# Optimization experiments

Hardware: AMD Instinct MI355X
Metric: run time of the kernel (lower is better)

The kernel has to match this reference:

```python
import jax, jax.numpy as jnp
import numpy as np

B, N, C, H = 2, 2048, 256, 8
HD = C // H
EPS = 1e-5


def _cdist(a, b):
    # a: (B,N,D), b: (B,M,D) -> (B,N,M) euclidean distance (torch.cdist p=2)
    d2 = (jnp.sum(a * a, -1)[:, :, None] + jnp.sum(b * b, -1)[:, None, :]
          - 2.0 * jnp.einsum('bnd,bmd->bnm', a, b))
    return jnp.sqrt(jnp.maximum(d2, 0.0))


def _ln(x, g, b):
    # LayerNorm over last axis
    m = jnp.mean(x, -1, keepdims=True)
    v = jnp.var(x, -1, keepdims=True)
    return (x - m) / jnp.sqrt(v + EPS) * g + b


def _conv1d(x, w, b=None):
    # 1x1 Conv1d: x (B,Cin,N), w (Cout,Cin)
    y = jnp.einsum('oc,bcn->bon', w, x)
    return y if b is None else y + b[:, None]


def setup_inputs() -> dict:
    key = jax.random.key(0)
    ks = jax.random.split(key, 32)
    s = 0.05
    inp = {
        'xyz_A': jax.random.normal(ks[0], (B, N, 3), jnp.float32),
        'featA': jax.random.normal(ks[1], (B, C, N), jnp.float32),
        'xyz_B': jax.random.normal(ks[2], (B, N, 3), jnp.float32),
        'featB': jax.random.normal(ks[3], (B, C, N), jnp.float32),
        # q/k/v projections (Conv1d 1x1)
        'qw': jax.random.normal(ks[4], (C, C), jnp.float32) * s,
        'qb': jnp.zeros((C,), jnp.float32),
        'kw': jax.random.normal(ks[5], (C, C), jnp.float32) * s,
        'kb': jnp.zeros((C,), jnp.float32),
        'vw': jax.random.normal(ks[6], (C, C), jnp.float32) * s,
        'vb': jnp.zeros((C,), jnp.float32),
        # spatial_bias_mlp: Conv2d(1,H/2,1,bias=False) -> BN2d(eval) -> ReLU -> Conv2d(H/2,H,1)
        'sbw1': jax.random.normal(ks[7], (H // 2,), jnp.float32) * s,
        'sbg': jnp.ones((H // 2,), jnp.float32),
        'sbb': jnp.zeros((H // 2,), jnp.float32),
        'sbm': jax.random.normal(ks[8], (H // 2,), jnp.float32) * 0.1,
        'sbv': jax.random.uniform(ks[9], (H // 2,), jnp.float32, 0.5, 1.5),
        'sbw2': jax.random.normal(ks[10], (H, H // 2), jnp.float32) * s,
        'sbb2': jnp.zeros((H,), jnp.float32),
        # dissimilarity projections
        'qdw': jax.random.normal(ks[11], (C, C), jnp.float32) * s,
        'qdb': jnp.zeros((C,), jnp.float32),
        'kdw': jax.random.normal(ks[12], (C, C), jnp.float32) * s,
        'kdb': jnp.zeros((C,), jnp.float32),
        # LayerNorms
        'lin_g': jnp.ones((C,), jnp.float32), 'lin_b': jnp.zeros((C,), jnp.float32),
        'lsim_g': jnp.ones((C,), jnp.float32), 'lsim_b': jnp.zeros((C,), jnp.float32),
        'ldis_g': jnp.ones((C,), jnp.float32), 'ldis_b': jnp.zeros((C,), jnp.float32),
        # fusion MLP: Conv1d(3C,2C,bias=False) -> BN1d(eval) -> ReLU -> Dropout(eval) -> Conv1d(2C,C)
        'fw1': jax.random.normal(ks[13], (2 * C, 3 * C), jnp.float32) * s,
        'fbg': jnp.ones((2 * C,), jnp.float32),
        'fbb': jnp.zeros((2 * C,), jnp.float32),
        'fbm': jax.random.normal(ks[14], (2 * C,), jnp.float32) * 0.1,
        'fbv': jax.random.uniform(ks[15], (2 * C,), jnp.float32, 0.5, 1.5),
        'fw2': jax.random.normal(ks[16], (C, 2 * C), jnp.float32) * s,
        'fb2': jnp.zeros((C,), jnp.float32),
    }
    return inp


def _forward(xyz_A, featA, xyz_B, featB, qw, qb, kw, kb, vw, vb,
             sbw1, sbg, sbb, sbm, sbv, sbw2, sbb2,
             qdw, qdb, kdw, kdb,
             lin_g, lin_b, lsim_g, lsim_b, ldis_g, ldis_b,
             fw1, fbg, fbb, fbm, fbv, fw2, fb2):
    # Pre-norm of featA over channels
    featA_norm = _ln(featA.transpose(0, 2, 1), lin_g, lin_b).transpose(0, 2, 1)  # (B,C,N)

    # Spatial bias: -cdist -> 1x1 conv (in_ch=1) -> BN(eval) -> ReLU -> 1x1 conv
    dist = _cdist(xyz_A, xyz_B)                                # (B,N,N)
    t = jnp.einsum('o,bnm->bonm', sbw1, -dist)                 # (B,H/2,N,N)
    t = (t - sbm[:, None, None]) / jnp.sqrt(sbv + EPS)[:, None, None]
    t = t * sbg[:, None, None] + sbb[:, None, None]
    t = jax.nn.relu(t)
    spatial_bias = jnp.einsum('oh,bhnm->bonm', sbw2, t) + sbb2[:, None, None]  # (B,H,N,N)

    # Similarity path
    q = _conv1d(featA_norm, qw, qb).reshape(B, H, HD, N).transpose(0, 1, 3, 2)  # (B,H,N,hd)
    k = _conv1d(featB, kw, kb).reshape(B, H, HD, N).transpose(0, 1, 3, 2)
    sim_scores = jnp.einsum('bhnd,bhmd->bhnm', q, k) / (HD ** 0.5) + spatial_bias

    # Dissimilarity path: feature cdist + spatial bias
    qd = _conv1d(featA_norm, qdw, qdb).transpose(0, 2, 1)      # (B,N,C)
    kd = _conv1d(featB, kdw, kdb).transpose(0, 2, 1)
    dissim_scores = _cdist(qd, kd)[:, None] + spatial_bias     # (B,H,N,N)

    sim_w = jax.nn.softmax(sim_scores, -1)
    dis_w = jax.nn.softmax(dissim_scores, -1)

    v = _conv1d(featB, vw, vb).reshape(B, H, HD, N).transpose(0, 1, 3, 2)       # (B,H,N,hd)
    ctx_sim = jnp.einsum('bhnm,bhmd->bhnd', sim_w, v).transpose(0, 1, 3, 2).reshape(B, C, N)
    ctx_sim = _ln(ctx_sim.transpose(0, 2, 1), lsim_g, lsim_b).transpose(0, 2, 1)
    ctx_dis = jnp.einsum('bhnm,bhmd->bhnd', dis_w, v).transpose(0, 1, 3, 2).reshape(B, C, N)
    ctx_dis = _ln(ctx_dis.transpose(0, 2, 1), ldis_g, ldis_b).transpose(0, 2, 1)

    fused = jnp.concatenate([featA_norm, ctx_sim, ctx_dis], axis=1)            # (B,3C,N)
    x = jnp.einsum('oc,bcn->bon', fw1, fused)
    x = (x - fbm[:, None]) / jnp.sqrt(fbv + EPS)[:, None] * fbg[:, None] + fbb[:, None]
    x = jax.nn.relu(x)  # Dropout is identity in eval mode
    out = _conv1d(x, fw2, fb2) + featA  # residual_proj is Identity (in==out)
    return out


def reference(xyz_A, featA, xyz_B, featB, qw, qb, kw, kb, vw, vb,
              sbw1, sbg, sbb, sbm, sbv, sbw2, sbb2,
              qdw, qdb, kdw, kdb,
              lin_g, lin_b, lsim_g, lsim_b, ldis_g, ldis_b,
              fw1, fbg, fbb, fbm, fbv, fw2, fb2):
    return _forward(xyz_A, featA, xyz_B, featB, qw, qb, kw, kb, vw, vb,
                    sbw1, sbg, sbb, sbm, sbv, sbw2, sbb2,
                    qdw, qdb, kdw, kdb,
                    lin_g, lin_b, lsim_g, lsim_b, ldis_g, ldis_b,
                    fw1, fbg, fbb, fbm, fbv, fw2, fb2)
```

## Files before the change

### kernel.cpp

```cpp
#include <hip/hip_runtime.h>

#define B_ 2
#define N_ 2048
#define C_ 256
#define H_ 8
#define HD_ 32
#define EPSf 1e-5f
#define LOG2E 1.4426950408889634f
#define THRv 8.0f

typedef __bf16   bf16x8 __attribute__((ext_vector_type(8)));
typedef float    f32x4  __attribute__((ext_vector_type(4)));
typedef _Float16 f16x4  __attribute__((ext_vector_type(4)));
typedef _Float16 f16x2  __attribute__((ext_vector_type(2)));

static constexpr size_t MB_ = 1024 * 1024;
static constexpr size_t OFF_FANT = 0;
static constexpr size_t OFF_FBT  = 2 * MB_;
static constexpr size_t OFF_QPK  = 4 * MB_;
static constexpr size_t OFF_KPK  = 6 * MB_;
static constexpr size_t OFF_VPK  = 8 * MB_;
static constexpr size_t OFF_QDT  = 10 * MB_;
static constexpr size_t OFF_KDT  = 12 * MB_;
static constexpr size_t OFF_QQ   = 14 * MB_;
static constexpr size_t OFF_KK   = 14 * MB_ + 16 * 1024;
static constexpr size_t OFF_FSD  = 14 * MB_ + 64 * 1024;
static constexpr size_t OFF_PART  = 47 * MB_;
static constexpr size_t OFF_STATM = 55 * MB_;
static constexpr size_t OFF_STATL = 56 * MB_;
static constexpr size_t OFF_CSLN  = 15 * MB_;
static constexpr size_t OFF_CDLN  = 17 * MB_;
static constexpr size_t OFF_X1T   = 19 * MB_;
static constexpr size_t WS_NEED   = 63 * MB_;

__device__ __forceinline__ float rfl(float x){
  return __uint_as_float(__builtin_amdgcn_readfirstlane(__float_as_uint(x)));
}
__device__ __forceinline__ float fexp2(float x){ return __builtin_amdgcn_exp2f(x); }
__device__ __forceinline__ bf16x8 cvt8(const float* p){
  float4 a = *reinterpret_cast<const float4*>(p);
  float4 c = *reinterpret_cast<const float4*>(p + 4);
  bf16x8 r;
  r[0]=(__bf16)a.x; r[1]=(__bf16)a.y; r[2]=(__bf16)a.z; r[3]=(__bf16)a.w;
  r[4]=(__bf16)c.x; r[5]=(__bf16)c.y; r[6]=(__bf16)c.z; r[7]=(__bf16)c.w;
  return r;
}
__device__ __forceinline__ unsigned int packh2(float lo, float hi){
  f16x2 h; h[0] = (_Float16)lo; h[1] = (_Float16)hi;
  return __builtin_bit_cast(unsigned int, h);
}
__device__ __forceinline__ void unpackh2(unsigned int u, float& lo, float& hi){
  f16x2 h = __builtin_bit_cast(f16x2, u);
  lo = (float)h[0]; hi = (float)h[1];
}
__device__ __forceinline__ f16x4 pack4(float a, float b, float c, float d){
  auto lo = __builtin_amdgcn_cvt_pkrtz(a, b);
  auto hi = __builtin_amdgcn_cvt_pkrtz(c, d);
  unsigned long long u = (unsigned long long)__builtin_bit_cast(unsigned int, lo)
      | ((unsigned long long)__builtin_bit_cast(unsigned int, hi) << 32);
  return __builtin_bit_cast(f16x4, u);
}

__global__ __launch_bounds__(256) void prep_kernel(const float* __restrict__ featA,
    const float* __restrict__ featB, __bf16* __restrict__ fanT, __bf16* __restrict__ fbT,
    const float* __restrict__ gam, const float* __restrict__ bet){
  int b = blockIdx.y;
  int t = threadIdx.x;
  __shared__ float sh[9536];
  if (blockIdx.x < 64){
    int n0 = blockIdx.x * 32;
    int nl = t & 31, cg = t >> 5;
    float* tile = sh;
    float* red1 = sh + 8448;
    float* red2 = red1 + 256;
    float* mus  = red2 + 256;
    float* rss  = mus + 32;
    float* gsh  = rss + 32;
    float* bsh  = gsh + 256;
    gsh[t] = gam[t]; bsh[t] = bet[t];
    #pragma unroll
    for (int i = 0; i < 32; i++){
      int c = cg * 32 + i;
      tile[c * 33 + nl] = featA[((size_t)(b * C_ + c)) * N_ + n0 + nl];
    }
    __syncthreads();
    float s1 = 0.f, s2 = 0.f;
    #pragma unroll
    for (int i = 0; i < 32; i++){
      float v = tile[(cg * 32 + i) * 33 + nl];
      s1 += v; s2 += v * v;
    }
    red1[cg * 32 + nl] = s1; red2[cg * 32 + nl] = s2;
    __syncthreads();
    if (t < 32){
      float a = 0.f, q = 0.f;
      #pragma unroll
      for (int i = 0; i < 8; i++){ a += red1[i * 32 + t]; q += red2[i * 32 + t]; }
      float m = a / (float)C_;
      mus[t] = m; rss[t] = rsqrtf(q / (float)C_ - m * m + EPSf);
    }
    __syncthreads();
    float mu = mus[nl], rs = rss[nl];
    size_t obase = ((size_t)(b * N_ + n0 + nl)) * C_;
    #pragma unroll
    for (int i = 0; i < 32; i++){
      int c = cg * 32 + i;
      fanT[obase + c] = (__bf16)((tile[c * 33 + nl] - mu) * rs * gsh[c] + bsh[c]);
    }
  } else {
    int idx = blockIdx.x - 64;
    int n0 = (idx & 31) * 64, c0 = (idx >> 5) * 64;
    float* tile = sh;
    int cl = t >> 6, nl = t & 63;
    #pragma unroll
    for (int i = 0; i < 16; i++)
      tile[(i * 4 + cl) * 65 + nl] = featB[((size_t)(b * C_ + c0 + i * 4 + cl)) * N_ + n0 + nl];
    __syncthreads();
    int nr = t >> 2, cc = (t & 3) * 16;
    alignas(16) __bf16 tmp[16];
    #pragma unroll
    for (int j = 0; j < 16; j++) tmp[j] = (__bf16)tile[(cc + j) * 65 + nr];
    size_t d = ((size_t)(b * N_ + n0 + nr)) * C_ + c0 + cc;
    *reinterpret_cast<uint4*>(&fbT[d])     = *reinterpret_cast<uint4*>(&tmp[0]);
    *reinterpret_cast<uint4*>(&fbT[d + 8]) = *reinterpret_cast<uint4*>(&tmp[8]);
  }
}

__global__ __launch_bounds__(256) void proj_mfma(const __bf16* __restrict__ fanT,
    const __bf16* __restrict__ fbT, __bf16* __restrict__ wsh,
    const float* __restrict__ qw, const float* __restrict__ qb,
    const float* __restrict__ kw, const float* __restrict__ kb,
    const float* __restrict__ vw, const float* __restrict__ vb,
    const float* __restrict__ qdw, const float* __restrict__ qdb,
    const float* __restrict__ kdw, const float* __restrict__ kdb){
  const int p = blockIdx.z % 5, b = blockIdx.z / 5;
  const int t = threadIdx.x, w = t >> 6, lane = t & 63, ln = lane & 15, g = lane >> 4;
  const float *W, *bias;
  const __bf16* X;
  __bf16* Y;
  if (p == 0)      { W = qw;  bias = qb;  X = fanT; Y = wsh + (OFF_QPK - OFF_FANT) / 2; }
  else if (p == 1) { W = kw;  bias = kb;  X = fbT;  Y = wsh + (OFF_KPK - OFF_FANT) / 2; }
  else if (p == 2) { W = vw;  bias = vb;  X = fbT;  Y = wsh + (OFF_VPK - OFF_FANT) / 2; }
  else if (p == 3) { W = qdw; bias = qdb; X = fanT; Y = wsh + (OFF_QDT - OFF_FANT) / 2; }
  else             { W = kdw; bias = kdb; X = fbT;  Y = wsh + (OFF_KDT - OFF_FANT) / 2; }

  f32x4 acc[4];
  #pragma unroll
  for (int i = 0; i < 4; i++) acc[i] = (f32x4){0.f, 0.f, 0.f, 0.f};

  if (p != 2){
    const int n0w = blockIdx.x * 64 + w * 16, o0 = blockIdx.y * 64;
    #pragma unroll
    for (int ks = 0; ks < 8; ks++){
      bf16x8 af = *reinterpret_cast<const bf16x8*>(
          &X[((size_t)(b * N_ + n0w + ln)) * C_ + ks * 32 + g * 8]);
      #pragma unroll
      for (int ot = 0; ot < 4; ot++){
        bf16x8 bf = cvt8(&W[(size_t)(o0 + ot * 16 + ln) * C_ + ks * 32 + g * 8]);
        acc[ot] = __builtin_amdgcn_mfma_f32_16x16x32_bf16(af, bf, acc[ot], 0, 0, 0);
      }
    }
    const float inv = 0.17677669529663687f * LOG2E;
    #pragma unroll
    for (int ot = 0; ot < 4; ot++){
      int o = o0 + ot * 16 + ln;
      float bz = bias[o];
      #pragma unroll
      for (int r = 0; r < 4; r++){
        int n = n0w + g * 4 + r;
        float val = acc[ot][r] + bz;
        if (p == 0){
          val *= inv;
          Y[(((size_t)(b * H_ + (o >> 5))) * N_ + n) * HD_ + (o & 31)] = (__bf16)val;
        } else if (p == 1){
          Y[(((size_t)(b * H_ + (o >> 5))) * N_ + n) * HD_ + (o & 31)] = (__bf16)val;
        } else {
          Y[((size_t)(b * N_ + n)) * C_ + o] = (__bf16)val;
        }
      }
    }
  } else {
    const int o0w = blockIdx.y * 64 + w * 16, n0 = blockIdx.x * 64;
    #pragma unroll
    for (int ks = 0; ks < 8; ks++){
      bf16x8 af = cvt8(&W[(size_t)(o0w + ln) * C_ + ks * 32 + g * 8]);
      #pragma unroll
      for (int nt = 0; nt < 4; nt++){
        bf16x8 bf = *reinterpret_cast<const bf16x8*>(
            &X[((size_t)(b * N_ + n0 + nt * 16 + ln)) * C_ + ks * 32 + g * 8]);
        acc[nt] = __builtin_amdgcn_mfma_f32_16x16x32_bf16(af, bf, acc[nt], 0, 0, 0);
      }
    }
    float bz[4];
    #pragma unroll
    for (int r = 0; r < 4; r++) bz[r] = vb[o0w + g * 4 + r];
    #pragma unroll
    for (int nt = 0; nt < 4; nt++)
      #pragma unroll
      for (int r = 0; r < 4; r++){
        int o = o0w + g * 4 + r, n = n0 + nt * 16 + ln;
        size_t idx = ((size_t)(b * C_ + o)) * N_ + n;
        ((_Float16*)Y)[idx] = (_Float16)(acc[nt][r] + bz[r]);
      }
  }
}

__global__ __launch_bounds__(256) void norms_b(const __bf16* __restrict__ qdT,
    const __bf16* __restrict__ kdT, float* __restrict__ qq, float* __restrict__ kk){
  int b = blockIdx.y, n = blockIdx.x * 64 + (threadIdx.x >> 2), part = threadIdx.x & 3;
  size_t base = ((size_t)(b * N_ + n)) * C_ + part * 64;
  float s1 = 0.f, s2 = 0.f;
  #pragma unroll
  for (int i = 0; i < 8; i++){
    bf16x8 a = *reinterpret_cast<const bf16x8*>(&qdT[base + i * 8]);
    bf16x8 d = *reinterpret_cast<const bf16x8*>(&kdT[base + i * 8]);
    #pragma unroll
    for (int j = 0; j < 8; j++){
      float fa = (float)a[j]; s1 += fa * fa;
      float fd = (float)d[j]; s2 += fd * fd;
    }
  }
  s1 += __shfl_xor(s1, 1); s1 += __shfl_xor(s1, 2);
  s2 += __shfl_xor(s2, 1); s2 += __shfl_xor(s2, 2);
  if (part == 0){ qq[b * N_ + n] = s1; kk[b * N_ + n] = s2; }
}

__global__ __launch_bounds__(256) void pairdist_mfma(const __bf16* __restrict__ qdT,
    const __bf16* __restrict__ kdT, const float* __restrict__ qq,
    const float* __restrict__ kk, const float* __restrict__ xyzA,
    const float* __restrict__ xyzB, unsigned int* __restrict__ fsd){
  const int t = threadIdx.x, w = t >> 6, lane = t & 63, ln = lane & 15, g = lane >> 4;
  const int b = blockIdx.z, n0 = blockIdx.y * 64, n0w = n0 + w * 16, m0 = blockIdx.x * 64;
  __shared__ float4 xa[64], xb[64];
  __shared__ unsigned int sbl[4][16][68];

  if (t < 64){
    const float* p = &xyzA[((size_t)(b * N_ + n0 + t)) * 3];
    xa[t] = make_float4(p[0], p[1], p[2], 0.f);
  } else if (t < 128){
    const float* p = &xyzB[((size_t)(b * N_ + m0 + t - 64)) * 3];
    xb[t - 64] = make_float4(p[0], p[1], p[2], 0.f);
  }
  bf16x8 qfr[8];
  #pragma unroll
  for (int ks = 0; ks < 8; ks++)
    qfr[ks] = *reinterpret_cast<const bf16x8*>(
        &qdT[((size_t)(b * N_ + n0w + ln)) * C_ + ks * 32 + g * 8]);
  float qqv[4];
  #pragma unroll
  for (int r = 0; r < 4; r++) qqv[r] = qq[b * N_ + n0w + g * 4 + r];
  __syncthreads();
  float4 xav[4];
  #pragma unroll
  for (int r = 0; r < 4; r++) xav[r] = xa[w * 16 + g * 4 + r];

  #pragma unroll
  for (int mt = 0; mt < 4; mt++){
    f32x4 a = (f32x4){0.f, 0.f, 0.f, 0.f};
    #pragma unroll
    for (int ks = 0; ks < 8; ks++){
      bf16x8 kfr = *reinterpret_cast<const bf16x8*>(
          &kdT[((size_t)(b * N_ + m0 + mt * 16 + ln)) * C_ + ks * 32 + g * 8]);
      a = __builtin_amdgcn_mfma_f32_16x16x32_bf16(qfr[ks], kfr, a, 0, 0, 0);
    }
    float kkv = kk[b * N_ + m0 + mt * 16 + ln];
    float4 xbv = xb[mt * 16 + ln];
    #pragma unroll
    for (int r = 0; r < 4; r++){
      float d2 = qqv[r] + kkv - 2.f * a[r];
      float fd = sqrtf(fmaxf(d2, 0.f)) * LOG2E;
      float dx = xav[r].x - xbv.x, dy = xav[r].y - xbv.y, dz = xav[r].z - xbv.z;
      float sd = sqrtf(dx * dx + dy * dy + dz * dz);
      sbl[w][g * 4 + r][mt * 16 + ln] = packh2(fd, sd);
    }
  }
  #pragma unroll
  for (int it = 0; it < 4; it++){
    int row = it * 4 + (lane >> 4), cq = lane & 15;
    uint4 v = *reinterpret_cast<const uint4*>(&sbl[w][row][cq * 4]);
    *reinterpret_cast<uint4*>(&fsd[((size_t)(b * N_ + n0w + row)) * N_ + m0 + cq * 4]) = v;
  }
}

struct TileRegs { uint4 fu[4]; bf16x8 kf[4]; };

__device__ __forceinline__ void load_tile(TileRegs& T, const __bf16* kbase,
    const unsigned int* fsdrow, int m0, int ln, int g){
  #pragma unroll
  for (int mt = 0; mt < 4; mt++){
    T.fu[mt] = *reinterpret_cast<const uint4*>(&fsdrow[m0 + mt * 16 + g * 4]);
    T.kf[mt] = *reinterpret_cast<const bf16x8*>(&kbase[(size_t)(m0 + mt * 16 + ln) * HD_ + g * 8]);
  }
}

__device__ __forceinline__ void compute_tile7(const TileRegs& T,
    const _Float16* vbase, int m0, int ln, int g, bf16x8 qf,
    const float* Ac, const float* Bc, const float* W2h, float C0,
    f32x4* os, f32x4* od, float& ms, float& lps, float& md, float& lpd){
  f32x4 sa[4];
  #pragma unroll
  for (int mt = 0; mt < 4; mt++){
    f32x4 z = (f32x4){0.f, 0.f, 0.f, 0.f};
    sa[mt] = __builtin_amdgcn_mfma_f32_16x16x32_bf16(T.kf[mt], qf, z, 0, 0, 0);
  }
  f16x4 vf[2][4];
  #pragma unroll
  for (int mt = 0; mt < 4; mt++)
    #pragma unroll
    for (int dt = 0; dt < 2; dt++)
      vf[dt][mt] = *reinterpret_cast<const f16x4*>(
          &vbase[(size_t)(dt * 16 + ln) * N_ + m0 + mt * 16 + g * 4]);
  f16x4 pAs[4], pAd[4];
  float tss = 0.f, tsd = 0.f, mxs = -3e38f, mxd = -3e38f;
  #pragma unroll
  for (int mt = 0; mt < 4; mt++){
    float ps[4], pd[4];
    #pragma unroll
    for (int r = 0; r < 4; r++){
      unsigned int uu = (r == 0) ? T.fu[mt].x : (r == 1) ? T.fu[mt].y
                      : (r == 2) ? T.fu[mt].z : T.fu[mt].w;
      float fdl, sd;
      unpackh2(uu, fdl, sd);
      float u0 = fmaxf(fmaf(Ac[0], sd, Bc[0]), 0.f);
      float u1 = fmaxf(fmaf(Ac[1], sd, Bc[1]), 0.f);
      float u2 = fmaxf(fmaf(Ac[2], sd, Bc[2]), 0.f);
      float u3 = fmaxf(fmaf(Ac[3], sd, Bc[3]), 0.f);
      float bias = fmaf(W2h[0], u0, fmaf(W2h[1], u1, fmaf(W2h[2], u2, fmaf(W2h[3], u3, C0))));
      float s = sa[mt][r] + bias;
      float d = fdl + bias;
      mxs = fmaxf(mxs, s); mxd = fmaxf(mxd, d);
      ps[r] = fexp2(s - ms); pd[r] = fexp2(d - md);
      tss += ps[r]; tsd += pd[r];
    }
    pAs[mt] = pack4(ps[0], ps[1], ps[2], ps[3]);
    pAd[mt] = pack4(pd[0], pd[1], pd[2], pd[3]);
  }
  bool fs  = !__all(mxs <= ms + THRv);
  bool fdp = !__all(mxd <= md + THRv);
  if (fs || fdp){
    if (fs){
      float mr = fmaxf(mxs, __shfl_xor(mxs, 16));
      mr = fmaxf(mr, __shfl_xor(mr, 32));
      float nms = fmaxf(ms, mr);
      float f = fexp2(ms - nms);
      ms = nms; lps *= f;
      float a0 = __shfl(f, g * 4 + 0), a1 = __shfl(f, g * 4 + 1);
      float a2 = __shfl(f, g * 4 + 2), a3 = __shfl(f, g * 4 + 3);
      #pragma unroll
      for (int dt = 0; dt < 2; dt++){
        os[dt][0] *= a0; os[dt][1] *= a1; os[dt][2] *= a2; os[dt][3] *= a3;
      }
    }
    if (fdp){
      float mr = fmaxf(mxd, __shfl_xor(mxd, 16));
      mr = fmaxf(mr, __shfl_xor(mr, 32));
      float nmd = fmaxf(md, mr);
      float f = fexp2(md - nmd);
      md = nmd; lpd *= f;
      float a0 = __shfl(f, g * 4 + 0), a1 = __shfl(f, g * 4 + 1);
      float a2 = __shfl(f, g * 4 + 2), a3 = __shfl(f, g * 4 + 3);
      #pragma unroll
      for (int dt = 0; dt < 2; dt++){
        od[dt][0] *= a0; od[dt][1] *= a1; od[dt][2] *= a2; od[dt][3] *= a3;
      }
    }
    tss = 0.f; tsd = 0.f;
    #pragma unroll
    for (int mt = 0; mt < 4; mt++){
      float ps[4], pd[4];
      #pragma unroll
      for (int r = 0; r < 4; r++){
        unsigned int uu = (r == 0) ? T.fu[mt].x : (r == 1) ? T.fu[mt].y
                        : (r == 2) ? T.fu[mt].z : T.fu[mt].w;
        float fdl, sd;
        unpackh2(uu, fdl, sd);
        float u0 = fmaxf(fmaf(Ac[0], sd, Bc[0]), 0.f);
        float u1 = fmaxf(fmaf(Ac[1], sd, Bc[1]), 0.f);
        float u2 = fmaxf(fmaf(Ac[2], sd, Bc[2]), 0.f);
        float u3 = fmaxf(fmaf(Ac[3], sd, Bc[3]), 0.f);
        float bias = fmaf(W2h[0], u0, fmaf(W2h[1], u1, fmaf(W2h[2], u2, fmaf(W2h[3], u3, C0))));
        float s = sa[mt][r] + bias;
        float d = fdl + bias;
        ps[r] = fexp2(s - ms); pd[r] = fexp2(d - md);
        tss += ps[r]; tsd += pd[r];
      }
      pAs[mt] = pack4(ps[0], ps[1], ps[2], ps[3]);
      pAd[mt] = pack4(pd[0], pd[1], pd[2], pd[3]);
    }
  }
  lps += tss; lpd += tsd;
  #pragma unroll
  for (int mt = 0; mt < 4; mt++)
    #pragma unroll
    for (int dt = 0; dt < 2; dt++){
      os[dt] = __builtin_amdgcn_mfma_f32_16x16x16f16(pAs[mt], vf[dt][mt], os[dt], 0, 0, 0);
      od[dt] = __builtin_amdgcn_mfma_f32_16x16x16f16(pAd[mt], vf[dt][mt], od[dt], 0, 0, 0);
    }
}

__global__ __launch_bounds__(256, 4) void dual_attn7(
    const __bf16* __restrict__ qpk, const __bf16* __restrict__ kpk,
    const _Float16* __restrict__ vph, const unsigned int* __restrict__ fsd,
    const float* __restrict__ sbw1, const float* __restrict__ sbg, const float* __restrict__ sbb,
    const float* __restrict__ sbm, const float* __restrict__ sbv,
    const float* __restrict__ sbw2, const float* __restrict__ sbb2,
    _Float16* __restrict__ partO, float* __restrict__ statM, float* __restrict__ statL){
  const int t = threadIdx.x, w = t >> 6, lane = t & 63, ln = lane & 15, g = lane >> 4;
  const int h = blockIdx.y;
  const int b = blockIdx.z >> 1, split = blockIdx.z & 1;
  const int nbase = blockIdx.x * 64 + w * 16;
  const int n = nbase + ln;
  const int mstart = split * (N_ / 2);

  float Ac[4], Bc[4], W2h[4];
  #pragma unroll
  for (int j = 0; j < 4; j++){
    float rs = rsqrtf(sbv[j] + EPSf);
    Ac[j]  = rfl(-sbw1[j] * rs * sbg[j]);
    Bc[j]  = rfl(-sbm[j] * rs * sbg[j] + sbb[j]);
    W2h[j] = rfl(sbw2[h * 4 + j]) * LOG2E;
  }
  float C0 = rfl(sbb2[h]) * LOG2E;

  bf16x8 qf = *reinterpret_cast<const bf16x8*>(
      &qpk[(((size_t)(b * H_ + h)) * N_ + n) * HD_ + g * 8]);
  const unsigned int* fsdrow = &fsd[((size_t)(b * N_ + n)) * N_];
  const __bf16* kbase = &kpk[(((size_t)(b * H_ + h)) * N_) * HD_];
  const _Float16* vbase = &vph[((size_t)(b * C_ + h * HD_)) * N_];

  f32x4 os[2], od[2];
  #pragma unroll
  for (int i = 0; i < 2; i++){ os[i] = (f32x4){0.f,0.f,0.f,0.f}; od[i] = (f32x4){0.f,0.f,0.f,0.f}; }
  float ms = -3e38f, lps = 0.f, md = -3e38f, lpd = 0.f;

  TileRegs T;
  for (int i = 0; i < 16; i++){
    int m0 = mstart + i * 64;
    load_tile(T, kbase, fsdrow, m0, ln, g);
    compute_tile7(T, vbase, m0, ln, g, qf, Ac, Bc, W2h, C0, os, od, ms, lps, md, lpd);
  }

  lps += __shfl_xor(lps, 16); lps += __shfl_xor(lps, 32);
  lpd += __shfl_xor(lpd, 16); lpd += __shfl_xor(lpd, 32);
  float is = 1.f / lps, idd = 1.f / lpd;
  float isr[4], idr[4];
  #pragma unroll
  for (int r = 0; r < 4; r++){
    isr[r] = __shfl(is, g * 4 + r);
    idr[r] = __shfl(idd, g * 4 + r);
  }
  #pragma unroll
  for (int dt = 0; dt < 2; dt++)
    #pragma unroll
    for (int r = 0; r < 4; r++){
      int nn = nbase + g * 4 + r;
      int ch = h * HD_ + dt * 16 + ln;
      size_t p0 = (((size_t)(0 * 2 + split) * B_ + b) * N_ + nn) * C_ + ch;
      size_t p1 = (((size_t)(2 + split) * B_ + b) * N_ + nn) * C_ + ch;
      partO[p0] = (_Float16)(os[dt][r] * isr[r]);
      partO[p1] = (_Float16)(od[dt][r] * idr[r]);
    }
  if (lane < 16){
    int nn = nbase + lane;
    size_t s0 = (((size_t)(0 * 2 + split) * B_ + b) * H_ + h) * N_ + nn;
    size_t s1 = (((size_t)(2 + split) * B_ + b) * H_ + h) * N_ + nn;
    statM[s0] = ms; statL[s0] = lps;
    statM[s1] = md; statL[s1] = lpd;
  }
}

__global__ __launch_bounds__(256) void combine_ln(
    const _Float16* __restrict__ partO, const float* __restrict__ statM,
    const float* __restrict__ statL, __bf16* __restrict__ csLN, __bf16* __restrict__ cdLN,
    const float* __restrict__ lsg, const float* __restrict__ lsb,
    const float* __restrict__ ldg, const float* __restrict__ ldb){
  const int path = blockIdx.y;
  const int w = threadIdx.x >> 6, lane = threadIdx.x & 63;
  const size_t row = (size_t)blockIdx.x * 4 + w;
  const int b = (int)(row >> 11), n = (int)(row & (N_ - 1));
  const int h = lane >> 3;
  const float* gg = path ? ldg : lsg;
  const float* bb = path ? ldb : lsb;
  __bf16* dst = path ? cdLN : csLN;

  size_t pb0 = (((size_t)(path * 2 + 0) * B_ + b) * N_ + n) * C_ + lane * 4;
  size_t pb1 = (((size_t)(path * 2 + 1) * B_ + b) * N_ + n) * C_ + lane * 4;
  f16x4 p0 = *reinterpret_cast<const f16x4*>(&partO[pb0]);
  f16x4 p1 = *reinterpret_cast<const f16x4*>(&partO[pb1]);
  size_t sb0 = (((size_t)(path * 2 + 0) * B_ + b) * H_ + h) * N_ + n;
  size_t sb1 = (((size_t)(path * 2 + 1) * B_ + b) * H_ + h) * N_ + n;
  float m0 = statM[sb0], l0 = statL[sb0];
  float m1 = statM[sb1], l1 = statL[sb1];
  float M = fmaxf(m0, m1);
  float w0 = l0 * fexp2(m0 - M), w1 = l1 * fexp2(m1 - M);
  float inv = 1.f / (w0 + w1);
  float o[4];
  #pragma unroll
  for (int j = 0; j < 4; j++)
    o[j] = (w0 * (float)p0[j] + w1 * (float)p1[j]) * inv;

  float s1 = o[0] + o[1] + o[2] + o[3];
  float s2 = o[0]*o[0] + o[1]*o[1] + o[2]*o[2] + o[3]*o[3];
  #pragma unroll
  for (int off = 1; off < 64; off <<= 1){
    s1 += __shfl_xor(s1, off);
    s2 += __shfl_xor(s2, off);
  }
  float mu = s1 / (float)C_;
  float rs = rsqrtf(s2 / (float)C_ - mu * mu + EPSf);
  float4 g4 = *reinterpret_cast<const float4*>(&gg[lane * 4]);
  float4 b4 = *reinterpret_cast<const float4*>(&bb[lane * 4]);
  alignas(8) __bf16 o4[4];
  o4[0] = (__bf16)((o[0] - mu) * rs * g4.x + b4.x);
  o4[1] = (__bf16)((o[1] - mu) * rs * g4.y + b4.y);
  o4[2] = (__bf16)((o[2] - mu) * rs * g4.z + b4.z);
  o4[3] = (__bf16)((o[3] - mu) * rs * g4.w + b4.w);
  *reinterpret_cast<uint2*>(&dst[row * C_ + lane * 4]) = *reinterpret_cast<uint2*>(o4);
}

__global__ __launch_bounds__(256) void fusion1_mfma(const __bf16* __restrict__ fanT,
    const __bf16* __restrict__ csLN, const __bf16* __restrict__ cdLN,
    __bf16* __restrict__ X1T, const float* __restrict__ fw1,
    const float* __restrict__ fbg, const float* __restrict__ fbb,
    const float* __restrict__ fbm, const float* __restrict__ fbv){
  const int t = threadIdx.x, w = t >> 6, lane = t & 63, ln = lane & 15, g = lane >> 4;
  const int b = blockIdx.z, o0 = blockIdx.y * 64, n0w = blockIdx.x * 64 + w * 16;
  f32x4 acc[4];
  #pragma unroll
  for (int i = 0; i < 4; i++) acc[i] = (f32x4){0.f, 0.f, 0.f, 0.f};
  const __bf16* segs[3] = {fanT, csLN, cdLN};
  #pragma unroll
  for (int ks = 0; ks < 24; ks++){
    const __bf16* base = segs[ks >> 3];
    int coff = (ks & 7) * 32 + g * 8;
    bf16x8 af = *reinterpret_cast<const bf16x8*>(
        &base[((size_t)(b * N_ + n0w + ln)) * C_ + coff]);
    #pragma unroll
    for (int ot = 0; ot < 4; ot++){
      bf16x8 bf = cvt8(&fw1[(size_t)(o0 + ot * 16 + ln) * (3 * C_) + ks * 32 + g * 8]);
      acc[ot] = __builtin_amdgcn_mfma_f32_16x16x32_bf16(af, bf, acc[ot], 0, 0, 0);
    }
  }
  #pragma unroll
  for (int ot = 0; ot < 4; ot++){
    int o = o0 + ot * 16 + ln;
    float mn = fbm[o], rs = rsqrtf(fbv[o] + EPSf), gg = fbg[o], be = fbb[o];
    #pragma unroll
    for (int r = 0; r < 4; r++){
      int n = n0w + g * 4 + r;
      float x = (acc[ot][r] - mn) * rs * gg + be;
      X1T[((size_t)(b * N_ + n)) * (2 * C_) + o] = (__bf16)fmaxf(x, 0.f);
    }
  }
}

__global__ __launch_bounds__(256) void fusion2_mfma(const __bf16* __restrict__ X1T,
    const float* __restrict__ fw2, const float* __restrict__ fb2,
    const float* __restrict__ featA, float* __restrict__ out){
  const int t = threadIdx.x, w = t >> 6, lane = t & 63, ln = lane & 15, g = lane >> 4;
  const int b = blockIdx.z, o0w = blockIdx.y * 64 + w * 16, n0 = blockIdx.x * 64;
  f32x4 acc[4];
  #pragma unroll
  for (int i = 0; i < 4; i++) acc[i] = (f32x4){0.f, 0.f, 0.f, 0.f};
  #pragma unroll
  for (int ks = 0; ks < 16; ks++){
    bf16x8 af = cvt8(&fw2[(size_t)(o0w + ln) * (2 * C_) + ks * 32 + g * 8]);
    #pragma unroll
    for (int nt = 0; nt < 4; nt++){
      bf16x8 bf = *reinterpret_cast<const bf16x8*>(
          &X1T[((size_t)(b * N_ + n0 + nt * 16 + ln)) * (2 * C_) + ks * 32 + g * 8]);
      acc[nt] = __builtin_amdgcn_mfma_f32_16x16x32_bf16(af, bf, acc[nt], 0, 0, 0);
    }
  }
  float bz[4];
  #pragma unroll
  for (int r = 0; r < 4; r++) bz[r] = fb2[o0w + g * 4 + r];
  #pragma unroll
  for (int nt = 0; nt < 4; nt++)
    #pragma unroll
    for (int r = 0; r < 4; r++){
      int o = o0w + g * 4 + r, n = n0 + nt * 16 + ln;
      size_t oi = ((size_t)(b * C_ + o)) * N_ + n;
      out[oi] = acc[nt][r] + bz[r] + featA[oi];
    }
}

extern "C" void kernel_launch(void* const* d_in, const int* in_sizes, int n_in,
                              void* d_out, int out_size, void* d_ws, size_t ws_size,
                              hipStream_t stream){
  (void)in_sizes; (void)n_in; (void)out_size;
  if (ws_size < WS_NEED) return;

  const float* xyzA  = (const float*)d_in[0];
  const float* featA = (const float*)d_in[1];
  const float* xyzB  = (const float*)d_in[2];
  const float* featB = (const float*)d_in[3];
  const float* qw  = (const float*)d_in[4];   const float* qb  = (const float*)d_in[5];
  const float* kw  = (const float*)d_in[6];   const float* kb  = (const float*)d_in[7];
  const float* vw  = (const float*)d_in[8];   const float* vb  = (const float*)d_in[9];
  const float* sbw1= (const float*)d_in[10];  const float* sbg = (const float*)d_in[11];
  const float* sbb = (const float*)d_in[12];  const float* sbm = (const float*)d_in[13];
  const float* sbv = (const float*)d_in[14];  const float* sbw2= (const float*)d_in[15];
  const float* sbb2= (const float*)d_in[16];
  const float* qdw = (const float*)d_in[17];  const float* qdb = (const float*)d_in[18];
  const float* kdw = (const float*)d_in[19];  const float* kdb = (const float*)d_in[20];
  const float* ling= (const float*)d_in[21];  const float* linb= (const float*)d_in[22];
  const float* lsg = (const float*)d_in[23];  const float* lsb = (const float*)d_in[24];
  const float* ldg = (const float*)d_in[25];  const float* ldb = (const float*)d_in[26];
  const float* fw1 = (const float*)d_in[27];  const float* fbg = (const float*)d_in[28];
  const float* fbb = (const float*)d_in[29];  const float* fbm = (const float*)d_in[30];
  const float* fbv = (const float*)d_in[31];  const float* fw2 = (const float*)d_in[32];
  const float* fb2 = (const float*)d_in[33];

  char* ws = (char*)d_ws;
  __bf16*   fanT = (__bf16*)(ws + OFF_FANT);
  __bf16*   fbT  = (__bf16*)(ws + OFF_FBT);
  __bf16*   qpk  = (__bf16*)(ws + OFF_QPK);
  __bf16*   kpk  = (__bf16*)(ws + OFF_KPK);
  _Float16* vph  = (_Float16*)(ws + OFF_VPK);
  __bf16*   qdT  = (__bf16*)(ws + OFF_QDT);
  __bf16*   kdT  = (__bf16*)(ws + OFF_KDT);
  float*    qq   = (float*)(ws + OFF_QQ);
  float*    kk   = (float*)(ws + OFF_KK);
  unsigned int* fsd = (unsigned int*)(ws + OFF_FSD);
  _Float16* partO = (_Float16*)(ws + OFF_PART);
  float*    statM = (float*)(ws + OFF_STATM);
  float*    statL = (float*)(ws + OFF_STATL);
  __bf16*   csLN  = (__bf16*)(ws + OFF_CSLN);
  __bf16*   cdLN  = (__bf16*)(ws + OFF_CDLN);
  __bf16*   X1T   = (__bf16*)(ws + OFF_X1T);
  float*    out   = (float*)d_out;

  prep_kernel<<<dim3(192, B_), 256, 0, stream>>>(featA, featB, fanT, fbT, ling, linb);
  proj_mfma<<<dim3(N_ / 64, C_ / 64, 5 * B_), 256, 0, stream>>>(
      fanT, fbT, fanT, qw, qb, kw, kb, vw, vb, qdw, qdb, kdw, kdb);
  norms_b<<<dim3(N_ / 64, B_), 256, 0, stream>>>(qdT, kdT, qq, kk);
  pairdist_mfma<<<dim3(N_ / 64, N_ / 64, B_), 256, 0, stream>>>(
      qdT, kdT, qq, kk, xyzA, xyzB, fsd);
  dual_attn7<<<dim3(N_ / 64, H_, B_ * 2), 256, 0, stream>>>(
      qpk, kpk, vph, fsd, sbw1, sbg, sbb, sbm, sbv, sbw2, sbb2,
      partO, statM, statL);
  combine_ln<<<dim3(B_ * N_ / 4, 2), 256, 0, stream>>>(
      partO, statM, statL, csLN, cdLN, lsg, lsb, ldg, ldb);
  fusion1_mfma<<<dim3(N_ / 64, (2 * C_) / 64, B_), 256, 0, stream>>>(
      fanT, csLN, cdLN, X1T, fw1, fbg, fbb, fbm, fbv);
  fusion2_mfma<<<dim3(N_ / 64, C_ / 64, B_), 256, 0, stream>>>(
      X1T, fw2, fb2, featA, out);
}
```

Baseline: 282.8 us.

## Process two heads per attention block to share pair-distance loads and bias MLP

The dual attention kernel now handles two heads per thread block instead of one, so each fsd tile (packed feature distance and spatial distance) is loaded once and the spatial-bias MLP's shared ReLU terms are computed once for both heads. The grid's head dimension is halved and launch bounds drop to 2 blocks per SM to leave room for the doubled register state. This is meant to cut global traffic on the large N×N fsd buffer and redundant ALU work. In exchange, register pressure and per-block work rise and occupancy falls, which could reduce latency hiding.

Result: faster. 253.7 us, median of 2 (-10.3%).

```diff
diff --git a/kernel.cpp b/kernel.cpp
--- a/kernel.cpp
+++ b/kernel.cpp
@@ -282,123 +282,7 @@
   }
 }
 
-struct TileRegs { uint4 fu[4]; bf16x8 kf[4]; };
-
-__device__ __forceinline__ void load_tile(TileRegs& T, const __bf16* kbase,
-    const unsigned int* fsdrow, int m0, int ln, int g){
-  #pragma unroll
-  for (int mt = 0; mt < 4; mt++){
-    T.fu[mt] = *reinterpret_cast<const uint4*>(&fsdrow[m0 + mt * 16 + g * 4]);
-    T.kf[mt] = *reinterpret_cast<const bf16x8*>(&kbase[(size_t)(m0 + mt * 16 + ln) * HD_ + g * 8]);
-  }
-}
-
-__device__ __forceinline__ void compute_tile7(const TileRegs& T,
-    const _Float16* vbase, int m0, int ln, int g, bf16x8 qf,
-    const float* Ac, const float* Bc, const float* W2h, float C0,
-    f32x4* os, f32x4* od, float& ms, float& lps, float& md, float& lpd){
-  f32x4 sa[4];
-  #pragma unroll
-  for (int mt = 0; mt < 4; mt++){
-    f32x4 z = (f32x4){0.f, 0.f, 0.f, 0.f};
-    sa[mt] = __builtin_amdgcn_mfma_f32_16x16x32_bf16(T.kf[mt], qf, z, 0, 0, 0);
-  }
-  f16x4 vf[2][4];
-  #pragma unroll
-  for (int mt = 0; mt < 4; mt++)
-    #pragma unroll
-    for (int dt = 0; dt < 2; dt++)
-      vf[dt][mt] = *reinterpret_cast<const f16x4*>(
-          &vbase[(size_t)(dt * 16 + ln) * N_ + m0 + mt * 16 + g * 4]);
-  f16x4 pAs[4], pAd[4];
-  float tss = 0.f, tsd = 0.f, mxs = -3e38f, mxd = -3e38f;
-  #pragma unroll
-  for (int mt = 0; mt < 4; mt++){
-    float ps[4], pd[4];
-    #pragma unroll
-    for (int r = 0; r < 4; r++){
-      unsigned int uu = (r == 0) ? T.fu[mt].x : (r == 1) ? T.fu[mt].y
-                      : (r == 2) ? T.fu[mt].z : T.fu[mt].w;
-      float fdl, sd;
-      unpackh2(uu, fdl, sd);
-      float u0 = fmaxf(fmaf(Ac[0], sd, Bc[0]), 0.f);
-      float u1 = fmaxf(fmaf(Ac[1], sd, Bc[1]), 0.f);
-      float u2 = fmaxf(fmaf(Ac[2], sd, Bc[2]), 0.f);
-      float u3 = fmaxf(fmaf(Ac[3], sd, Bc[3]), 0.f);
-      float bias = fmaf(W2h[0], u0, fmaf(W2h[1], u1, fmaf(W2h[2], u2, fmaf(W2h[3], u3, C0))));
-      float s = sa[mt][r] + bias;
-      float d = fdl + bias;
-      mxs = fmaxf(mxs, s); mxd = fmaxf(mxd, d);
-      ps[r] = fexp2(s - ms); pd[r] = fexp2(d - md);
-      tss += ps[r]; tsd += pd[r];
-    }
-    pAs[mt] = pack4(ps[0], ps[1], ps[2], ps[3]);
-    pAd[mt] = pack4(pd[0], pd[1], pd[2], pd[3]);
-  }
-  bool fs  = !__all(mxs <= ms + THRv);
-  bool fdp = !__all(mxd <= md + THRv);
-  if (fs || fdp){
-    if (fs){
-      float mr = fmaxf(mxs, __shfl_xor(mxs, 16));
-      mr = fmaxf(mr, __shfl_xor(mr, 32));
-      float nms = fmaxf(ms, mr);
-      float f = fexp2(ms - nms);
-      ms = nms; lps *= f;
-      float a0 = __shfl(f, g * 4 + 0), a1 = __shfl(f, g * 4 + 1);
-      float a2 = __shfl(f, g * 4 + 2), a3 = __shfl(f, g * 4 + 3);
-      #pragma unroll
-      for (int dt = 0; dt < 2; dt++){
-        os[dt][0] *= a0; os[dt][1] *= a1; os[dt][2] *= a2; os[dt][3] *= a3;
-      }
-    }
-    if (fdp){
-      float mr = fmaxf(mxd, __shfl_xor(mxd, 16));
-      mr = fmaxf(mr, __shfl_xor(mr, 32));
-      float nmd = fmaxf(md, mr);
-      float f = fexp2(md - nmd);
-      md = nmd; lpd *= f;
-      float a0 = __shfl(f, g * 4 + 0), a1 = __shfl(f, g * 4 + 1);
-      float a2 = __shfl(f, g * 4 + 2), a3 = __shfl(f, g * 4 + 3);
-      #pragma unroll
-      for (int dt = 0; dt < 2; dt++){
-        od[dt][0] *= a0; od[dt][1] *= a1; od[dt][2] *= a2; od[dt][3] *= a3;
-      }
-    }
-    tss = 0.f; tsd = 0.f;
-    #pragma unroll
-    for (int mt = 0; mt < 4; mt++){
-      float ps[4], pd[4];
-      #pragma unroll
-      for (int r = 0; r < 4; r++){
-        unsigned int uu = (r == 0) ? T.fu[mt].x : (r == 1) ? T.fu[mt].y
-                        : (r == 2) ? T.fu[mt].z : T.fu[mt].w;
-        float fdl, sd;
-        unpackh2(uu, fdl, sd);
-        float u0 = fmaxf(fmaf(Ac[0], sd, Bc[0]), 0.f);
-        float u1 = fmaxf(fmaf(Ac[1], sd, Bc[1]), 0.f);
-        float u2 = fmaxf(fmaf(Ac[2], sd, Bc[2]), 0.f);
-        float u3 = fmaxf(fmaf(Ac[3], sd, Bc[3]), 0.f);
-        float bias = fmaf(W2h[0], u0, fmaf(W2h[1], u1, fmaf(W2h[2], u2, fmaf(W2h[3], u3, C0))));
-        float s = sa[mt][r] + bias;
-        float d = fdl + bias;
-        ps[r] = fexp2(s - ms); pd[r] = fexp2(d - md);
-        tss += ps[r]; tsd += pd[r];
-      }
-      pAs[mt] = pack4(ps[0], ps[1], ps[2], ps[3]);
-      pAd[mt] = pack4(pd[0], pd[1], pd[2], pd[3]);
-    }
-  }
-  lps += tss; lpd += tsd;
-  #pragma unroll
-  for (int mt = 0; mt < 4; mt++)
-    #pragma unroll
-    for (int dt = 0; dt < 2; dt++){
-      os[dt] = __builtin_amdgcn_mfma_f32_16x16x16f16(pAs[mt], vf[dt][mt], os[dt], 0, 0, 0);
-      od[dt] = __builtin_amdgcn_mfma_f32_16x16x16f16(pAd[mt], vf[dt][mt], od[dt], 0, 0, 0);
-    }
-}
-
-__global__ __launch_bounds__(256, 4) void dual_attn7(
+__global__ __launch_bounds__(256, 2) void dual_attn8(
     const __bf16* __restrict__ qpk, const __bf16* __restrict__ kpk,
     const _Float16* __restrict__ vph, const unsigned int* __restrict__ fsd,
     const float* __restrict__ sbw1, const float* __restrict__ sbg, const float* __restrict__ sbb,
@@ -406,66 +290,218 @@
     const float* __restrict__ sbw2, const float* __restrict__ sbb2,
     _Float16* __restrict__ partO, float* __restrict__ statM, float* __restrict__ statL){
   const int t = threadIdx.x, w = t >> 6, lane = t & 63, ln = lane & 15, g = lane >> 4;
-  const int h = blockIdx.y;
+  const int h0 = blockIdx.y * 2, h1 = h0 + 1;
   const int b = blockIdx.z >> 1, split = blockIdx.z & 1;
   const int nbase = blockIdx.x * 64 + w * 16;
   const int n = nbase + ln;
   const int mstart = split * (N_ / 2);
 
-  float Ac[4], Bc[4], W2h[4];
+  float Ac[4], Bc[4], W20[4], W21[4];
   #pragma unroll
   for (int j = 0; j < 4; j++){
     float rs = rsqrtf(sbv[j] + EPSf);
     Ac[j]  = rfl(-sbw1[j] * rs * sbg[j]);
     Bc[j]  = rfl(-sbm[j] * rs * sbg[j] + sbb[j]);
-    W2h[j] = rfl(sbw2[h * 4 + j]) * LOG2E;
-  }
-  float C0 = rfl(sbb2[h]) * LOG2E;
-
-  bf16x8 qf = *reinterpret_cast<const bf16x8*>(
-      &qpk[(((size_t)(b * H_ + h)) * N_ + n) * HD_ + g * 8]);
+    W20[j] = rfl(sbw2[h0 * 4 + j]) * LOG2E;
+    W21[j] = rfl(sbw2[h1 * 4 + j]) * LOG2E;
+  }
+  float C00 = rfl(sbb2[h0]) * LOG2E;
+  float C01 = rfl(sbb2[h1]) * LOG2E;
+
+  bf16x8 qf0 = *reinterpret_cast<const bf16x8*>(
+      &qpk[(((size_t)(b * H_ + h0)) * N_ + n) * HD_ + g * 8]);
+  bf16x8 qf1 = *reinterpret_cast<const bf16x8*>(
+      &qpk[(((size_t)(b * H_ + h1)) * N_ + n) * HD_ + g * 8]);
   const unsigned int* fsdrow = &fsd[((size_t)(b * N_ + n)) * N_];
-  const __bf16* kbase = &kpk[(((size_t)(b * H_ + h)) * N_) * HD_];
-  const _Float16* vbase = &vph[((size_t)(b * C_ + h * HD_)) * N_];
-
-  f32x4 os[2], od[2];
-  #pragma unroll
-  for (int i = 0; i < 2; i++){ os[i] = (f32x4){0.f,0.f,0.f,0.f}; od[i] = (f32x4){0.f,0.f,0.f,0.f}; }
-  float ms = -3e38f, lps = 0.f, md = -3e38f, lpd = 0.f;
-
-  TileRegs T;
+  const __bf16* kb0 = &kpk[((size_t)(b * H_ + h0)) * N_ * HD_];
+  const __bf16* kb1 = &kpk[((size_t)(b * H_ + h1)) * N_ * HD_];
+  const _Float16* vb0 = &vph[((size_t)(b * C_ + h0 * HD_)) * N_];
+  const _Float16* vb1 = &vph[((size_t)(b * C_ + h1 * HD_)) * N_];
+
+  f32x4 os0[2], od0[2], os1[2], od1[2];
+  #pragma unroll
+  for (int i = 0; i < 2; i++){
+    os0[i] = (f32x4){0.f,0.f,0.f,0.f}; od0[i] = (f32x4){0.f,0.f,0.f,0.f};
+    os1[i] = (f32x4){0.f,0.f,0.f,0.f}; od1[i] = (f32x4){0.f,0.f,0.f,0.f};
+  }
+  float ms0 = -3e38f, lps0 = 0.f, md0 = -3e38f, lpd0 = 0.f;
+  float ms1 = -3e38f, lps1 = 0.f, md1 = -3e38f, lpd1 = 0.f;
+
   for (int i = 0; i < 16; i++){
-    int m0 = mstart + i * 64;
-    load_tile(T, kbase, fsdrow, m0, ln, g);
-    compute_tile7(T, vbase, m0, ln, g, qf, Ac, Bc, W2h, C0, os, od, ms, lps, md, lpd);
-  }
-
-  lps += __shfl_xor(lps, 16); lps += __shfl_xor(lps, 32);
-  lpd += __shfl_xor(lpd, 16); lpd += __shfl_xor(lpd, 32);
-  float is = 1.f / lps, idd = 1.f / lpd;
-  float isr[4], idr[4];
+    const int m0 = mstart + i * 64;
+    uint4 fu[4];
+    bf16x8 kf0[4], kf1[4];
+    #pragma unroll
+    for (int mt = 0; mt < 4; mt++){
+      fu[mt]  = *reinterpret_cast<const uint4*>(&fsdrow[m0 + mt * 16 + g * 4]);
+      kf0[mt] = *reinterpret_cast<const bf16x8*>(&kb0[(size_t)(m0 + mt * 16 + ln) * HD_ + g * 8]);
+      kf1[mt] = *reinterpret_cast<const bf16x8*>(&kb1[(size_t)(m0 + mt * 16 + ln) * HD_ + g * 8]);
+    }
+    f32x4 sa0[4], sa1[4];
+    #pragma unroll
+    for (int mt = 0; mt < 4; mt++){
+      f32x4 z = (f32x4){0.f, 0.f, 0.f, 0.f};
+      sa0[mt] = __builtin_amdgcn_mfma_f32_16x16x32_bf16(kf0[mt], qf0, z, 0, 0, 0);
+    }
+    #pragma unroll
+    for (int mt = 0; mt < 4; mt++){
+      f32x4 z = (f32x4){0.f, 0.f, 0.f, 0.f};
+      sa1[mt] = __builtin_amdgcn_mfma_f32_16x16x32_bf16(kf1[mt], qf1, z, 0, 0, 0);
+    }
+    f16x4 vf0[2][4], vf1[2][4];
+    #pragma unroll
+    for (int mt = 0; mt < 4; mt++)
+      #pragma unroll
+      for (int dt = 0; dt < 2; dt++){
+        vf0[dt][mt] = *reinterpret_cast<const f16x4*>(
+            &vb0[(size_t)(dt * 16 + ln) * N_ + m0 + mt * 16 + g * 4]);
+        vf1[dt][mt] = *reinterpret_cast<const f16x4*>(
+            &vb1[(size_t)(dt * 16 + ln) * N_ + m0 + mt * 16 + g * 4]);
+      }
+
+    f16x4 pAs0[4], pAd0[4], pAs1[4], pAd1[4];
+    float tss0 = 0.f, tsd0 = 0.f, tss1 = 0.f, tsd1 = 0.f;
+    float mxs0 = -3e38f, mxd0 = -3e38f, mxs1 = -3e38f, mxd1 = -3e38f;
+    #pragma unroll
+    for (int mt = 0; mt < 4; mt++){
+      float ps0[4], pd0[4], ps1[4], pd1[4];
+      #pragma unroll
+      for (int r = 0; r < 4; r++){
+        unsigned int uu = (r == 0) ? fu[mt].x : (r == 1) ? fu[mt].y
+                        : (r == 2) ? fu[mt].z : fu[mt].w;
+        float fdl, sd;
+        unpackh2(uu, fdl, sd);
+        float u0 = fmaxf(fmaf(Ac[0], sd, Bc[0]), 0.f);
+        float u1 = fmaxf(fmaf(Ac[1], sd, Bc[1]), 0.f);
+        float u2 = fmaxf(fmaf(Ac[2], sd, Bc[2]), 0.f);
+        float u3 = fmaxf(fmaf(Ac[3], sd, Bc[3]), 0.f);
+        float b0 = fmaf(W20[0], u0, fmaf(W20[1], u1, fmaf(W20[2], u2, fmaf(W20[3], u3, C00))));
+        float b1 = fmaf(W21[0], u0, fmaf(W21[1], u1, fmaf(W21[2], u2, fmaf(W21[3], u3, C01))));
+        float s0 = sa0[mt][r] + b0, d0 = fdl + b0;
+        float s1 = sa1[mt][r] + b1, d1 = fdl + b1;
+        mxs0 = fmaxf(mxs0, s0); mxd0 = fmaxf(mxd0, d0);
+        mxs1 = fmaxf(mxs1, s1); mxd1 = fmaxf(mxd1, d1);
+        ps0[r] = fexp2(s0 - ms0); pd0[r] = fexp2(d0 - md0);
+        ps1[r] = fexp2(s1 - ms1); pd1[r] = fexp2(d1 - md1);
+        tss0 += ps0[r]; tsd0 += pd0[r]; tss1 += ps1[r]; tsd1 += pd1[r];
+      }
+      pAs0[mt] = pack4(ps0[0], ps0[1], ps0[2], ps0[3]);
+      pAd0[mt] = pack4(pd0[0], pd0[1], pd0[2], pd0[3]);
+      pAs1[mt] = pack4(ps1[0], ps1[1], ps1[2], ps1[3]);
+      pAd1[mt] = pack4(pd1[0], pd1[1], pd1[2], pd1[3]);
+    }
+    bool f0 = !__all(mxs0 <= ms0 + THRv);
+    bool f1 = !__all(mxd0 <= md0 + THRv);
+    bool f2 = !__all(mxs1 <= ms1 + THRv);
+    bool f3 = !__all(mxd1 <= md1 + THRv);
+    if (f0 || f1 || f2 || f3){
+      if (f0){
+        float mr = fmaxf(mxs0, __shfl_xor(mxs0, 16)); mr = fmaxf(mr, __shfl_xor(mr, 32));
+        float nm = fmaxf(ms0, mr), f = fexp2(ms0 - nm);
+        ms0 = nm; lps0 *= f;
+        float a0 = __shfl(f, g*4+0), a1 = __shfl(f, g*4+1), a2 = __shfl(f, g*4+2), a3 = __shfl(f, g*4+3);
+        #pragma unroll
+        for (int dt = 0; dt < 2; dt++){ os0[dt][0]*=a0; os0[dt][1]*=a1; os0[dt][2]*=a2; os0[dt][3]*=a3; }
+      }
+      if (f1){
+        float mr = fmaxf(mxd0, __shfl_xor(mxd0, 16)); mr = fmaxf(mr, __shfl_xor(mr, 32));
+        float nm = fmaxf(md0, mr), f = fexp2(md0 - nm);
+        md0 = nm; lpd0 *= f;
+        float a0 = __shfl(f, g*4+0), a1 = __shfl(f, g*4+1), a2 = __shfl(f, g*4+2), a3 = __shfl(f, g*4+3);
+        #pragma unroll
+        for (int dt = 0; dt < 2; dt++){ od0[dt][0]*=a0; od0[dt][1]*=a1; od0[dt][2]*=a2; od0[dt][3]*=a3; }
+      }
+      if (f2){
+        float mr = fmaxf(mxs1, __shfl_xor(mxs1, 16)); mr = fmaxf(mr, __shfl_xor(mr, 32));
+        float nm = fmaxf(ms1, mr), f = fexp2(ms1 - nm);
+        ms1 = nm; lps1 *= f;
+        float a0 = __shfl(f, g*4+0), a1 = __shfl(f, g*4+1), a2 = __shfl(f, g*4+2), a3 = __shfl(f, g*4+3);
+        #pragma unroll
+        for (int dt = 0; dt < 2; dt++){ os1[dt][0]*=a0; os1[dt][1]*=a1; os1[dt][2]*=a2; os1[dt][3]*=a3; }
+      }
+      if (f3){
+        float mr = fmaxf(mxd1, __shfl_xor(mxd1, 16)); mr = fmaxf(mr, __shfl_xor(mr, 32));
+        float nm = fmaxf(md1, mr), f = fexp2(md1 - nm);
+        md1 = nm; lpd1 *= f;
+        float a0 = __shfl(f, g*4+0), a1 = __shfl(f, g*4+1), a2 = __shfl(f, g*4+2), a3 = __shfl(f, g*4+3);
+        #pragma unroll
+        for (int dt = 0; dt < 2; dt++){ od1[dt][0]*=a0; od1[dt][1]*=a1; od1[dt][2]*=a2; od1[dt][3]*=a3; }
+      }
+      tss0 = 0.f; tsd0 = 0.f; tss1 = 0.f; tsd1 = 0.f;
+      #pragma unroll
+      for (int mt = 0; mt < 4; mt++){
+        float ps0[4], pd0[4], ps1[4], pd1[4];
+        #pragma unroll
+        for (int r = 0; r < 4; r++){
+          unsigned int uu = (r == 0) ? fu[mt].x : (r == 1) ? fu[mt].y
+                          : (r == 2) ? fu[mt].z : fu[mt].w;
+          float fdl, sd;
+          unpackh2(uu, fdl, sd);
+          float u0 = fmaxf(fmaf(Ac[0], sd, Bc[0]), 0.f);
+          float u1 = fmaxf(fmaf(Ac[1], sd, Bc[1]), 0.f);
+          float u2 = fmaxf(fmaf(Ac[2], sd, Bc[2]), 0.f);
+          float u3 = fmaxf(fmaf(Ac[3], sd, Bc[3]), 0.f);
+          float b0 = fmaf(W20[0], u0, fmaf(W20[1], u1, fmaf(W20[2], u2, fmaf(W20[3], u3, C00))));
+          float b1 = fmaf(W21[0], u0, fmaf(W21[1], u1, fmaf(W21[2], u2, fmaf(W21[3], u3, C01))));
+          ps0[r] = fexp2(sa0[mt][r] + b0 - ms0); pd0[r] = fexp2(fdl + b0 - md0);
+          ps1[r] = fexp2(sa1[mt][r] + b1 - ms1); pd1[r] = fexp2(fdl + b1 - md1);
+          tss0 += ps0[r]; tsd0 += pd0[r]; tss1 += ps1[r]; tsd1 += pd1[r];
+        }
+        pAs0[mt] = pack4(ps0[0], ps0[1], ps0[2], ps0[3]);
+        pAd0[mt] = pack4(pd0[0], pd0[1], pd0[2], pd0[3]);
+        pAs1[mt] = pack4(ps1[0], ps1[1], ps1[2], ps1[3]);
+        pAd1[mt] = pack4(pd1[0], pd1[1], pd1[2], pd1[3]);
+      }
+    }
+    lps0 += tss0; lpd0 += tsd0; lps1 += tss1; lpd1 += tsd1;
+    #pragma unroll
+    for (int mt = 0; mt < 4; mt++)
+      #pragma unroll
+      for (int dt = 0; dt < 2; dt++){
+        os0[dt] = __builtin_amdgcn_mfma_f32_16x16x16f16(pAs0[mt], vf0[dt][mt], os0[dt], 0, 0, 0);
+        od0[dt] = __builtin_amdgcn_mfma_f32_16x16x16f16(pAd0[mt], vf0[dt][mt], od0[dt], 0, 0, 0);
+        os1[dt] = __builtin_amdgcn_mfma_f32_16x16x16f16(pAs1[mt], vf1[dt][mt], os1[dt], 0, 0, 0);
+        od1[dt] = __builtin_amdgcn_mfma_f32_16x16x16f16(pAd1[mt], vf1[dt][mt], od1[dt], 0, 0, 0);
+      }
+  }
+
+  lps0 += __shfl_xor(lps0, 16); lps0 += __shfl_xor(lps0, 32);
+  lpd0 += __shfl_xor(lpd0, 16); lpd0 += __shfl_xor(lpd0, 32);
+  lps1 += __shfl_xor(lps1, 16); lps1 += __shfl_xor(lps1, 32);
+  lpd1 += __shfl_xor(lpd1, 16); lpd1 += __shfl_xor(lpd1, 32);
+  float is0 = 1.f / lps0, id0 = 1.f / lpd0, is1 = 1.f / lps1, id1 = 1.f / lpd1;
+  float is0r[4], id0r[4], is1r[4], id1r[4];
   #pragma unroll
   for (int r = 0; r < 4; r++){
-    isr[r] = __shfl(is, g * 4 + r);
-    idr[r] = __shfl(idd, g * 4 + r);
+    is0r[r] = __shfl(is0, g * 4 + r);
+    id0r[r] = __shfl(id0, g * 4 + r);
+    is1r[r] = __shfl(is1, g * 4 + r);
+    id1r[r] = __shfl(id1, g * 4 + r);
   }
   #pragma unroll
   for (int dt = 0; dt < 2; dt++)
     #pragma unroll
     for (int r = 0; r < 4; r++){
       int nn = nbase + g * 4 + r;
-      int ch = h * HD_ + dt * 16 + ln;
-      size_t p0 = (((size_t)(0 * 2 + split) * B_ + b) * N_ + nn) * C_ + ch;
-      size_t p1 = (((size_t)(2 + split) * B_ + b) * N_ + nn) * C_ + ch;
-      partO[p0] = (_Float16)(os[dt][r] * isr[r]);
-      partO[p1] = (_Float16)(od[dt][r] * idr[r]);
+      size_t rbase = (((size_t)split * B_ + b) * N_ + nn) * C_;
+      size_t rbase2 = (((size_t)(2 + split) * B_ + b) * N_ + nn) * C_;
+      int ch0 = h0 * HD_ + dt * 16 + ln;
+      int ch1 = h1 * HD_ + dt * 16 + ln;
+      partO[rbase  + ch0] = (_Float16)(os0[dt][r] * is0r[r]);
+      partO[rbase2 + ch0] = (_Float16)(od0[dt][r] * id0r[r]);
+      partO[rbase  + ch1] = (_Float16)(os1[dt][r] * is1r[r]);
+      partO[rbase2 + ch1] = (_Float16)(od1[dt][r] * id1r[r]);
     }
   if (lane < 16){
     int nn = nbase + lane;
-    size_t s0 = (((size_t)(0 * 2 + split) * B_ + b) * H_ + h) * N_ + nn;
-    size_t s1 = (((size_t)(2 + split) * B_ + b) * H_ + h) * N_ + nn;
-    statM[s0] = ms; statL[s0] = lps;
-    statM[s1] = md; statL[s1] = lpd;
+    size_t s00 = (((size_t)split * B_ + b) * H_ + h0) * N_ + nn;
+    size_t s10 = (((size_t)(2 + split) * B_ + b) * H_ + h0) * N_ + nn;
+    size_t s01 = (((size_t)split * B_ + b) * H_ + h1) * N_ + nn;
+    size_t s11 = (((size_t)(2 + split) * B_ + b) * H_ + h1) * N_ + nn;
+    statM[s00] = ms0; statL[s00] = lps0;
+    statM[s10] = md0; statL[s10] = lpd0;
+    statM[s01] = ms1; statL[s01] = lps1;
+    statM[s11] = md1; statL[s11] = lpd1;
   }
 }
 
@@ -637,7 +673,7 @@
   norms_b<<<dim3(N_ / 64, B_), 256, 0, stream>>>(qdT, kdT, qq, kk);
   pairdist_mfma<<<dim3(N_ / 64, N_ / 64, B_), 256, 0, stream>>>(
       qdT, kdT, qq, kk, xyzA, xyzB, fsd);
-  dual_attn7<<<dim3(N_ / 64, H_, B_ * 2), 256, 0, stream>>>(
+  dual_attn8<<<dim3(N_ / 64, H_ / 2, B_ * 2), 256, 0, stream>>>(
       qpk, kpk, vph, fsd, sbw1, sbg, sbb, sbm, sbv, sbw2, sbb2,
       partO, statM, statL);
   combine_ln<<<dim3(B_ * N_ / 4, 2), 256, 0, stream>>>(
```
